# Kernel tuning notes

Measured on AMD Instinct MI355X. Metric: run time of the kernel, lower is better.

Reference implementation:

```python
import jax, jax.numpy as jnp
import numpy as np

T, N, D, E, L = 3, 50000, 64, 800000, 2


def setup_inputs() -> dict:
    key = jax.random.key(0)
    ks = jax.random.split(key, 12)
    glorot = lambda k, shape: jax.random.uniform(
        k, shape, jnp.float32, -1.0, 1.0) * np.sqrt(6.0 / (shape[-2] + shape[-1]))
    return {
        "x": jax.random.normal(ks[0], (N, D), jnp.float32),
        "edge_index": jax.random.randint(ks[1], (2, E), 0, N),
        "edge_type": jax.random.randint(ks[2], (E,), 0, T),
        "edge_feature": jax.random.normal(ks[3], (T, D), jnp.float32),
        # per-layer parameters stacked along leading L axis
        "theta_g": glorot(ks[4], (L, T, D)),
        "theta_hi": glorot(ks[5], (L, T, D)),
        "theta_hj": glorot(ks[6], (L, T, D)),
        "we": glorot(ks[7], (L, D, D)),
        "wr": glorot(ks[8], (L, D, D)),
    }


def _scatter_softmax(r, row, n):
    # r: [T,E], softmax over edges grouped by destination node `row`
    rT = r.T  # [E,T]
    m = jax.ops.segment_max(rT, row, num_segments=n)  # [N,T]
    e = jnp.exp(rT - m[row])
    s = jax.ops.segment_sum(e, row, num_segments=n)
    return (e / s[row]).T  # [T,E]


def _layer(x, ef, tg, thi, thj, we, wr, row, col, etype, n):
    # attention logits per edge, per type-slice
    r_g = jnp.einsum('ed,td->te', ef, tg)[:, etype]          # [T,E]
    r_hi = jnp.einsum('tnd,td->tn', x, thi)[:, row]          # [T,E]
    r_hj = jnp.einsum('tnd,td->tn', x, thj)[:, col]          # [T,E]
    r = _scatter_softmax(r_g + r_hi + r_hj, row, n)          # [T,E]
    ef_new = ef @ wr                                         # [et,D]
    v = jax.nn.sigmoid(ef_new)[etype][None] * (x @ we)[:, col]  # [T,E,D]
    out = r[..., None] * v                                   # [T,E,D]
    out = jax.ops.segment_sum(out.transpose(1, 0, 2), row, num_segments=n)
    return out.transpose(1, 0, 2), ef_new                    # [T,N,D]


def reference(x, edge_index, edge_type, edge_feature, theta_g, theta_hi, theta_hj, we, wr):
    row, col = edge_index[0], edge_index[1]
    h = jnp.broadcast_to(x[None], (T, N, D))
    ef = edge_feature
    for i in range(L):
        h_prev = h
        out, ef = _layer(h, ef, theta_g[i], theta_hi[i], theta_hj[i],
                         we[i], wr[i], row, col, edge_type, N)
        if i == L - 1:
            h = out
            break
        h = h_prev + jax.nn.relu(out)  # dropout p=0 -> identity
        ef = jax.nn.relu(ef)
    return h
```

## Files before the change

kernel.cpp:

```cpp
#include <hip/hip_runtime.h>
#include <math.h>

#define TT 3
#define NN 50000
#define DD 64
#define EE 800000
#define LL 2
#define NK3 (NN * TT)
#define NB3 ((NK3 + 255) / 256)
#define CH 96
#define NBC ((EE + 255) / 256)
#define NBM ((NN + 63) / 64)

typedef _Float16 h4 __attribute__((ext_vector_type(4)));
typedef float f4 __attribute__((ext_vector_type(4)));

__global__ __launch_bounds__(256) void k_fusedA(
    const int* __restrict__ row, const int* __restrict__ et,
    int* __restrict__ counts, unsigned* __restrict__ keyrank,
    const float* __restrict__ x,
    const float* __restrict__ we,
    const float* __restrict__ thj,
    _Float16* __restrict__ hw0,
    float* __restrict__ ahj0,
    const float* __restrict__ ef0,
    const float* __restrict__ tg,
    const float* __restrict__ wr,
    float* __restrict__ rg,
    float* __restrict__ sig,
    _Float16* __restrict__ bf)
{
    __shared__ _Float16 Ah[64][68];
    __shared__ _Float16 Bt[80][68];
    int b = blockIdx.x, tid = threadIdx.x;

    if (b < NBC) {
        int e = b * 256 + tid;
        if (e < EE) {
            int key = row[e] * 3 + et[e];
            int r = atomicAdd(&counts[key], 1);
            keyrank[e] = ((unsigned)key << 14) | (unsigned)r;
        }
        return;
    }
    if (b < NBC + NBM) {
        long rbase = (long)(b - NBC) * 64;
        #pragma unroll
        for (int it = 0; it < 4; ++it) {
            int flat = (tid + it * 256) * 4;
            int r = flat >> 6, k = flat & 63;
            h4 hv = {};
            if (rbase + r < NN) {
                float4 v = *(const float4*)&x[(rbase + r) * 64 + k];
                hv = h4{ (_Float16)v.x, (_Float16)v.y, (_Float16)v.z, (_Float16)v.w };
            }
            *(h4*)&Ah[r][k] = hv;
        }
        for (int idx = tid; idx < 80 * 64; idx += 256) {
            int c = idx >> 6, k = idx & 63;
            float v = 0.f;
            if (c < 64) v = we[k * 64 + c];
            else if (c < 67) v = thj[(c - 64) * 64 + k];
            Bt[c][k] = (_Float16)v;
        }
        __syncthreads();
        int wid = tid >> 6, lane = tid & 63;
        int r16 = lane & 15, kq = lane >> 4;
        f4 acc[5] = {};
        #pragma unroll
        for (int ks = 0; ks < 4; ++ks) {
            int k0 = ks * 16 + kq * 4;
            h4 a = *(h4*)&Ah[wid * 16 + r16][k0];
            #pragma unroll
            for (int ct = 0; ct < 5; ++ct) {
                h4 bb = *(h4*)&Bt[ct * 16 + r16][k0];
                acc[ct] = __builtin_amdgcn_mfma_f32_16x16x16f16(a, bb, acc[ct], 0, 0, 0);
            }
        }
        #pragma unroll
        for (int j = 0; j < 4; ++j) {
            long g = rbase + wid * 16 + kq * 4 + j;
            if (g < NN) {
                #pragma unroll
                for (int ct = 0; ct < 4; ++ct)
                    hw0[g * 64 + ct * 16 + r16] = (_Float16)acc[ct][j];
                if (r16 < 3) ahj0[g * 4 + r16] = acc[4][j];
            }
        }
        return;
    }
    float* ef_l = (float*)&Ah[0][0];
    float* efn  = ef_l + TT * DD;
    for (int l = 0; l < LL; ++l)
        for (int idx = tid; idx < 80 * 64; idx += 256) {
            int c = idx >> 6, k = idx & 63;
            float v = 0.f;
            if (c < 64) v = we[l * 4096 + k * 64 + c];
            else if (c < 67) v = thj[l * 192 + (c - 64) * 64 + k];
            bf[l * 5120 + idx] = (_Float16)v;
        }
    if (tid < TT * DD) ef_l[tid] = ef0[tid];
    __syncthreads();
    for (int layer = 0; layer < LL; ++layer) {
        if (tid < TT * TT) {
            int t = tid / TT, tau = tid % TT;
            float s = 0.f;
            #pragma unroll
            for (int k = 0; k < DD; ++k)
                s += ef_l[tau * DD + k] * tg[layer * TT * DD + t * DD + k];
            rg[layer * TT * TT + tid] = s;
        }
        if (tid < TT * DD) {
            int tau = tid / DD, d = tid % DD;
            float s = 0.f;
            #pragma unroll
            for (int k = 0; k < DD; ++k)
                s += ef_l[tau * DD + k] * wr[layer * DD * DD + k * DD + d];
            efn[tid] = s;
            sig[layer * TT * DD + tid] = 1.f / (1.f + expf(-s));
        }
        __syncthreads();
        if (tid < TT * DD) ef_l[tid] = fmaxf(efn[tid], 0.f);
        __syncthreads();
    }
}

__global__ void k_bsum(const int* __restrict__ counts, int* __restrict__ bsum)
{
    __shared__ int red[256];
    int i = blockIdx.x * 256 + threadIdx.x;
    red[threadIdx.x] = (i < NK3) ? counts[i] : 0;
    __syncthreads();
    for (int off = 128; off >= 1; off >>= 1) {
        if (threadIdx.x < off) red[threadIdx.x] += red[threadIdx.x + off];
        __syncthreads();
    }
    if (threadIdx.x == 0) bsum[blockIdx.x] = red[0];
}

__global__ void k_emit2(const int* __restrict__ counts,
                        const int* __restrict__ bsum,
                        int* __restrict__ csroff)
{
    __shared__ int s[256];
    __shared__ int bpre_s;
    int b = blockIdx.x, tid = threadIdx.x;
    int pp = 0;
    for (int i = tid; i < b; i += 256) pp += bsum[i];
    s[tid] = pp;
    __syncthreads();
    for (int off = 128; off >= 1; off >>= 1) {
        if (tid < off) s[tid] += s[tid + off];
        __syncthreads();
    }
    if (tid == 0) bpre_s = s[0];
    __syncthreads();
    int bpre = bpre_s;
    int idx = b * 256 + tid;
    int c = (idx < NK3) ? counts[idx] : 0;
    s[tid] = c;
    __syncthreads();
    for (int off = 1; off < 256; off <<= 1) {
        int u = (tid >= off) ? s[tid - off] : 0;
        __syncthreads();
        s[tid] += u;
        __syncthreads();
    }
    if (idx < NK3) csroff[idx] = bpre + s[tid] - c;
    if (b == NB3 - 1 && tid == 255) csroff[NK3] = bpre + s[255];
}

__global__ void k_scatter3r(const unsigned* __restrict__ keyrank,
                            const int* __restrict__ col,
                            const int* __restrict__ csroff,
                            unsigned short* __restrict__ pk)
{
    int e = blockIdx.x * 256 + threadIdx.x;
    if (e < EE) {
        unsigned kr = keyrank[e];
        int pos = csroff[kr >> 14] + (int)(kr & 16383u);
        pk[pos] = (unsigned short)col[e];
    }
}

__global__ __launch_bounds__(256) void k_mm1(
    const _Float16* __restrict__ h,
    const _Float16* __restrict__ Bf,
    _Float16* __restrict__ hw,
    float* __restrict__ ahj)
{
    __shared__ _Float16 Ah[64][68];
    __shared__ _Float16 Bt[80][68];
    int tid = threadIdx.x;
    long rbase = (long)blockIdx.x * 64;

    #pragma unroll
    for (int it = 0; it < 4; ++it) {
        int flat = (tid + it * 256) * 4;
        int r = flat >> 6, k = flat & 63;
        h4 hv = {};
        if (rbase + r < NK3) hv = *(const h4*)&h[(rbase + r) * 64 + k];
        *(h4*)&Ah[r][k] = hv;
    }
    for (int e4 = tid; e4 < 80 * 64 / 4; e4 += 256) {
        int idx = e4 * 4;
        *(h4*)&Bt[idx >> 6][idx & 63] = *(const h4*)&Bf[idx];
    }
    __syncthreads();

    int wid = tid >> 6, lane = tid & 63;
    int r16 = lane & 15, kq = lane >> 4;
    f4 acc[5] = {};
    #pragma unroll
    for (int ks = 0; ks < 4; ++ks) {
        int k0 = ks * 16 + kq * 4;
        h4 a = *(h4*)&Ah[wid * 16 + r16][k0];
        #pragma unroll
        for (int ct = 0; ct < 5; ++ct) {
            h4 b = *(h4*)&Bt[ct * 16 + r16][k0];
            acc[ct] = __builtin_amdgcn_mfma_f32_16x16x16f16(a, b, acc[ct], 0, 0, 0);
        }
    }
    #pragma unroll
    for (int j = 0; j < 4; ++j) {
        long g = rbase + wid * 16 + kq * 4 + j;
        if (g < NK3) {
            int t = (g >= 2L * NN) ? 2 : (g >= NN ? 1 : 0);
            long n = g - (long)t * NN;
            #pragma unroll
            for (int ct = 0; ct < 4; ++ct)
                hw[((size_t)n * 3 + t) * 64 + ct * 16 + r16] = (_Float16)acc[ct][j];
            if (r16 == t) ahj[n * 4 + t] = acc[4][j];
        }
    }
}

__global__ __launch_bounds__(256) void k_edge0(
    const int* __restrict__ off3,
    const unsigned short* __restrict__ pk,
    const float* __restrict__ rg_l,
    const float* __restrict__ sig_l,
    const float* __restrict__ ahj4,
    const _Float16* __restrict__ hw,
    const float* __restrict__ x,
    _Float16* __restrict__ outh)
{
    __shared__ uint4 ent[4][CH];
    int wid = threadIdx.x >> 6, lane = threadIdx.x & 63;
    int n = blockIdx.x * 4 + wid;
    int b3 = n * 3;
    int s0 = off3[b3], s1 = off3[b3 + 1], s2 = off3[b3 + 2], s3 = off3[b3 + 3];
    float r00 = rg_l[0], r01 = rg_l[1], r02 = rg_l[2];
    float r10 = rg_l[3], r11 = rg_l[4], r12 = rg_l[5];
    float r20 = rg_l[6], r21 = rg_l[7], r22 = rg_l[8];
    float sg0 = sig_l[lane], sg1 = sig_l[64 + lane], sg2 = sig_l[128 + lane];
    const char* hwb = (const char*)hw + (size_t)lane * 2;
    uint4* myent = ent[wid];
    float acc0 = 0.f, acc1 = 0.f, acc2 = 0.f;
    float ps0 = 0.f, ps1 = 0.f, ps2 = 0.f;

    for (int base = s0; base < s3; base += CH) {
        int cnt = s3 - base; if (cnt > CH) cnt = CH;
        for (int jj = lane; jj < cnt; jj += 64) {
            int ei = base + jj;
            int c = pk[ei];
            int tau = (ei >= s1) + (ei >= s2);
            float4 aj = *(const float4*)&ahj4[c * 4];
            float g0 = (tau == 0) ? r00 : ((tau == 1) ? r01 : r02);
            float g1 = (tau == 0) ? r10 : ((tau == 1) ? r11 : r12);
            float g2 = (tau == 0) ? r20 : ((tau == 1) ? r21 : r22);
            float p0 = __expf(g0 + aj.x);
            float p1 = __expf(g1 + aj.y);
            float p2 = __expf(g2 + aj.z);
            ps0 += p0; ps1 += p1; ps2 += p2;
            myent[jj] = make_uint4(((unsigned)c * 128u) | ((unsigned)tau << 26),
                                   __float_as_uint(p0), __float_as_uint(p1),
                                   __float_as_uint(p2));
        }
        asm volatile("s_waitcnt lgkmcnt(0)" ::: "memory");

#define AGG(J) { uint4 e = myent[J];                                           \
        unsigned ta = e.x >> 26;                                               \
        float sg = (ta == 0) ? sg0 : ((ta == 1) ? sg1 : sg2);                  \
        float sv = sg * (float)*(const _Float16*)(hwb + (e.x & 0x03FFFFFFu));  \
        acc0 = fmaf(__uint_as_float(e.y), sv, acc0);                           \
        acc1 = fmaf(__uint_as_float(e.z), sv, acc1);                           \
        acc2 = fmaf(__uint_as_float(e.w), sv, acc2); }
        int j = 0;
        for (; j + 4 <= cnt; j += 4) { AGG(j) AGG(j + 1) AGG(j + 2) AGG(j + 3) }
        for (; j < cnt; ++j) { AGG(j) }
#undef AGG
        asm volatile("s_waitcnt lgkmcnt(0)" ::: "memory");
    }
    #pragma unroll
    for (int off = 32; off >= 1; off >>= 1) {
        ps0 += __shfl_xor(ps0, off);
        ps1 += __shfl_xor(ps1, off);
        ps2 += __shfl_xor(ps2, off);
    }
    float o0 = 0.f, o1 = 0.f, o2 = 0.f;
    if (s3 > s0) { o0 = acc0 / ps0; o1 = acc1 / ps1; o2 = acc2 / ps2; }
    size_t oi = (size_t)n * 64 + lane;
    float xv = x[oi];
    outh[oi]                       = (_Float16)(xv + fmaxf(o0, 0.f));
    outh[oi + (size_t)NN * 64]     = (_Float16)(xv + fmaxf(o1, 0.f));
    outh[oi + (size_t)2 * NN * 64] = (_Float16)(xv + fmaxf(o2, 0.f));
}

__global__ __launch_bounds__(256) void k_edge1(
    const int* __restrict__ off3,
    const unsigned short* __restrict__ pk,
    const float* __restrict__ rg_l,
    const float* __restrict__ sig_l,
    const float* __restrict__ ahj4,
    const _Float16* __restrict__ hw,
    float* __restrict__ outf)
{
    __shared__ uint4 ent[4][CH];
    int wid = threadIdx.x >> 6, lane = threadIdx.x & 63;
    int n = blockIdx.x * 4 + wid;
    int b3 = n * 3;
    int s0 = off3[b3], s1 = off3[b3 + 1], s2 = off3[b3 + 2], s3 = off3[b3 + 3];
    float r00 = rg_l[0], r01 = rg_l[1], r02 = rg_l[2];
    float r10 = rg_l[3], r11 = rg_l[4], r12 = rg_l[5];
    float r20 = rg_l[6], r21 = rg_l[7], r22 = rg_l[8];
    float sg0 = sig_l[lane], sg1 = sig_l[64 + lane], sg2 = sig_l[128 + lane];
    const char* hwb = (const char*)hw + (size_t)lane * 2;
    uint4* myent = ent[wid];
    float acc0 = 0.f, acc1 = 0.f, acc2 = 0.f;
    float ps0 = 0.f, ps1 = 0.f, ps2 = 0.f;

    for (int base = s0; base < s3; base += CH) {
        int cnt = s3 - base; if (cnt > CH) cnt = CH;
        for (int jj = lane; jj < cnt; jj += 64) {
            int ei = base + jj;
            int c = pk[ei];
            int tau = (ei >= s1) + (ei >= s2);
            float4 aj = *(const float4*)&ahj4[c * 4];
            float g0 = (tau == 0) ? r00 : ((tau == 1) ? r01 : r02);
            float g1 = (tau == 0) ? r10 : ((tau == 1) ? r11 : r12);
            float g2 = (tau == 0) ? r20 : ((tau == 1) ? r21 : r22);
            float p0 = __expf(g0 + aj.x);
            float p1 = __expf(g1 + aj.y);
            float p2 = __expf(g2 + aj.z);
            ps0 += p0; ps1 += p1; ps2 += p2;
            myent[jj] = make_uint4(((unsigned)c * 384u) | ((unsigned)tau << 26),
                                   __float_as_uint(p0), __float_as_uint(p1),
                                   __float_as_uint(p2));
        }
        asm volatile("s_waitcnt lgkmcnt(0)" ::: "memory");

#define AGG(J) { uint4 e = myent[J];                                           \
        unsigned ta = e.x >> 26;                                               \
        float sg = (ta == 0) ? sg0 : ((ta == 1) ? sg1 : sg2);                  \
        const char* ptr = hwb + (e.x & 0x03FFFFFFu);                           \
        float v0 = (float)*(const _Float16*)(ptr);                             \
        float v1 = (float)*(const _Float16*)(ptr + 128);                       \
        float v2 = (float)*(const _Float16*)(ptr + 256);                       \
        acc0 = fmaf(__uint_as_float(e.y), sg * v0, acc0);                      \
        acc1 = fmaf(__uint_as_float(e.z), sg * v1, acc1);                      \
        acc2 = fmaf(__uint_as_float(e.w), sg * v2, acc2); }
        int j = 0;
        for (; j + 4 <= cnt; j += 4) { AGG(j) AGG(j + 1) AGG(j + 2) AGG(j + 3) }
        for (; j < cnt; ++j) { AGG(j) }
#undef AGG
        asm volatile("s_waitcnt lgkmcnt(0)" ::: "memory");
    }
    #pragma unroll
    for (int off = 32; off >= 1; off >>= 1) {
        ps0 += __shfl_xor(ps0, off);
        ps1 += __shfl_xor(ps1, off);
        ps2 += __shfl_xor(ps2, off);
    }
    float o0 = 0.f, o1 = 0.f, o2 = 0.f;
    if (s3 > s0) { o0 = acc0 / ps0; o1 = acc1 / ps1; o2 = acc2 / ps2; }
    size_t oi = (size_t)n * 64 + lane;
    outf[oi]                       = o0;
    outf[oi + (size_t)NN * 64]     = o1;
    outf[oi + (size_t)2 * NN * 64] = o2;
}

extern "C" void kernel_launch(void* const* d_in, const int* in_sizes, int n_in,
                              void* d_out, int out_size, void* d_ws, size_t ws_size,
                              hipStream_t stream)
{
    const float* x   = (const float*)d_in[0];
    const int*   ei  = (const int*)d_in[1];
    const int*   row = ei;
    const int*   col = ei + EE;
    const int*   et  = (const int*)d_in[2];
    const float* ef  = (const float*)d_in[3];
    const float* tg  = (const float*)d_in[4];
    const float* thj = (const float*)d_in[6];
    const float* we  = (const float*)d_in[7];
    const float* wr  = (const float*)d_in[8];
    float* out = (float*)d_out;
    _Float16* h1h = (_Float16*)d_out;

    _Float16* hw1 = (_Float16*)d_ws;
    _Float16* hw0 = hw1 + (size_t)NN * 3 * 64;
    float* ahj0 = (float*)(hw0 + (size_t)NN * 64);
    float* ahj1 = ahj0 + (size_t)NN * 4;
    float* rg   = ahj1 + (size_t)NN * 4;
    float* sig  = rg + LL * 9;
    _Float16* bfB = (_Float16*)(sig + LL * 192);
    int* counts3 = (int*)(bfB + LL * 5120);
    int* csroff3 = counts3 + NK3;
    int* bsum    = csroff3 + NK3 + 1;
    unsigned* keyrank = (unsigned*)(bsum + NB3);
    unsigned short* csrpk = (unsigned short*)(keyrank + EE);

    hipMemsetAsync(counts3, 0, NK3 * sizeof(int), stream);
    k_fusedA<<<NBC + NBM + 1, 256, 0, stream>>>(row, et, counts3, keyrank,
                                                x, we, thj, hw0, ahj0,
                                                ef, tg, wr, rg, sig, bfB);
    k_bsum<<<NB3, 256, 0, stream>>>(counts3, bsum);
    k_emit2<<<NB3, 256, 0, stream>>>(counts3, bsum, csroff3);
    k_scatter3r<<<(EE + 255) / 256, 256, 0, stream>>>(keyrank, col, csroff3, csrpk);
    k_edge0<<<NN / 4, 256, 0, stream>>>(csroff3, csrpk, rg, sig, ahj0, hw0,
                                        x, h1h);
    k_mm1<<<(NK3 + 63) / 64, 256, 0, stream>>>(h1h, bfB + 5120, hw1, ahj1);
    k_edge1<<<NN / 4, 256, 0, stream>>>(csroff3, csrpk, rg + 9, sig + 192,
                                        ahj1, hw1, out);
}
```

Before: 173.5 us.

## Replace global-atomic CSR build with two-level bucketed counting sort

Replaces the per-key global atomic counting, the block-sum scan and the rank-based scatter with a two-level radix-style sort. Edges are first bucketed by row/128 using shared-memory histograms and a transposed per-block offset table, then each bucket is locally sorted by (row,type) key in shared memory to emit CSR offsets and column indices. The intent is to avoid heavily contended global atomics and scattered writes. The cost is extra passes, serial in-block scans over 3125 blocks per bucket column, and the removal of the memset.

After: 170.3 us. About the same (-1.9%).

```diff
diff --git a/kernel.cpp b/kernel.cpp
--- a/kernel.cpp
+++ b/kernel.cpp
@@ -7,17 +7,19 @@
 #define EE 800000
 #define LL 2
 #define NK3 (NN * TT)
-#define NB3 ((NK3 + 255) / 256)
 #define CH 96
 #define NBC ((EE + 255) / 256)
 #define NBM ((NN + 63) / 64)
+#define NBKT ((NN + 127) / 128)
+#define KPB 384
+#define HP 3136
 
 typedef _Float16 h4 __attribute__((ext_vector_type(4)));
 typedef float f4 __attribute__((ext_vector_type(4)));
 
 __global__ __launch_bounds__(256) void k_fusedA(
     const int* __restrict__ row, const int* __restrict__ et,
-    int* __restrict__ counts, unsigned* __restrict__ keyrank,
+    int* __restrict__ blockHistT,
     const float* __restrict__ x,
     const float* __restrict__ we,
     const float* __restrict__ thj,
@@ -32,15 +34,18 @@
 {
     __shared__ _Float16 Ah[64][68];
     __shared__ _Float16 Bt[80][68];
+    __shared__ int lhist[NBKT];
     int b = blockIdx.x, tid = threadIdx.x;
 
     if (b < NBC) {
+        for (int i = tid; i < NBKT; i += 256) lhist[i] = 0;
+        __syncthreads();
         int e = b * 256 + tid;
-        if (e < EE) {
-            int key = row[e] * 3 + et[e];
-            int r = atomicAdd(&counts[key], 1);
-            keyrank[e] = ((unsigned)key << 14) | (unsigned)r;
-        }
+        int bkt = row[e] >> 7;
+        atomicAdd(&lhist[bkt], 1);
+        __syncthreads();
+        for (int i = tid; i < NBKT; i += 256)
+            blockHistT[(size_t)i * HP + b] = lhist[i];
         return;
     }
     if (b < NBC + NBM) {
@@ -125,61 +130,134 @@
     }
 }
 
-__global__ void k_bsum(const int* __restrict__ counts, int* __restrict__ bsum)
-{
-    __shared__ int red[256];
-    int i = blockIdx.x * 256 + threadIdx.x;
-    red[threadIdx.x] = (i < NK3) ? counts[i] : 0;
+__global__ __launch_bounds__(256) void k_colscan(
+    int* __restrict__ blockHistT, int* __restrict__ bucketTotal)
+{
+    __shared__ int sc[256];
+    __shared__ int carryB;
+    int j = blockIdx.x, tid = threadIdx.x;
+    int* colp = blockHistT + (size_t)j * HP;
+    if (tid == 0) carryB = 0;
+    __syncthreads();
+    for (int c0 = 0; c0 < NBC; c0 += 256) {
+        int b = c0 + tid;
+        int v = (b < NBC) ? colp[b] : 0;
+        sc[tid] = v;
+        __syncthreads();
+        for (int off = 1; off < 256; off <<= 1) {
+            int u = (tid >= off) ? sc[tid - off] : 0;
+            __syncthreads();
+            sc[tid] += u;
+            __syncthreads();
+        }
+        int cb = carryB;
+        if (b < NBC) colp[b] = cb + sc[tid] - v;
+        __syncthreads();
+        if (tid == 0) carryB = cb + sc[255];
+        __syncthreads();
+    }
+    if (tid == 0) bucketTotal[j] = carryB;
+}
+
+__global__ __launch_bounds__(256) void k_bucket(
+    const int* __restrict__ row, const int* __restrict__ et,
+    const int* __restrict__ col,
+    const int* __restrict__ bucketTotal,
+    const int* __restrict__ blockOffT,
+    unsigned* __restrict__ bucketed)
+{
+    __shared__ int lrank[NBKT];
+    __shared__ int lbase[NBKT];
+    __shared__ int sc[256];
+    __shared__ int carryC;
+    int b = blockIdx.x, tid = threadIdx.x;
+    for (int i = tid; i < NBKT; i += 256) lrank[i] = 0;
+    if (tid == 0) carryC = 0;
+    __syncthreads();
+    for (int c0 = 0; c0 < NBKT; c0 += 256) {
+        int i = c0 + tid;
+        int v = (i < NBKT) ? bucketTotal[i] : 0;
+        sc[tid] = v;
+        __syncthreads();
+        for (int off = 1; off < 256; off <<= 1) {
+            int u = (tid >= off) ? sc[tid - off] : 0;
+            __syncthreads();
+            sc[tid] += u;
+            __syncthreads();
+        }
+        int cb = carryC;
+        if (i < NBKT) lbase[i] = cb + sc[tid] - v;
+        __syncthreads();
+        if (tid == 0) carryC = cb + sc[255];
+        __syncthreads();
+    }
+    int e = b * 256 + tid;
+    int r = row[e], tt = et[e], c = col[e];
+    int bkt = r >> 7;
+    int kl = (r - (bkt << 7)) * 3 + tt;
+    int rk = atomicAdd(&lrank[bkt], 1);
+    int pos = lbase[bkt] + blockOffT[(size_t)bkt * HP + b] + rk;
+    bucketed[pos] = ((unsigned)kl << 16) | (unsigned)c;
+}
+
+__global__ __launch_bounds__(256) void k_emit3(
+    const unsigned* __restrict__ bucketed,
+    const int* __restrict__ bucketTotal,
+    int* __restrict__ csroff,
+    unsigned short* __restrict__ pk)
+{
+    __shared__ int counts[KPB];
+    __shared__ int csr[KPB];
+    __shared__ int sc[256];
+    __shared__ int carryS;
+    int j = blockIdx.x, tid = threadIdx.x;
+    int pp = 0;
+    for (int i = tid; i < j; i += 256) pp += bucketTotal[i];
+    sc[tid] = pp;
     __syncthreads();
     for (int off = 128; off >= 1; off >>= 1) {
-        if (threadIdx.x < off) red[threadIdx.x] += red[threadIdx.x + off];
-        __syncthreads();
-    }
-    if (threadIdx.x == 0) bsum[blockIdx.x] = red[0];
-}
-
-__global__ void k_emit2(const int* __restrict__ counts,
-                        const int* __restrict__ bsum,
-                        int* __restrict__ csroff)
-{
-    __shared__ int s[256];
-    __shared__ int bpre_s;
-    int b = blockIdx.x, tid = threadIdx.x;
-    int pp = 0;
-    for (int i = tid; i < b; i += 256) pp += bsum[i];
-    s[tid] = pp;
-    __syncthreads();
-    for (int off = 128; off >= 1; off >>= 1) {
-        if (tid < off) s[tid] += s[tid + off];
-        __syncthreads();
-    }
-    if (tid == 0) bpre_s = s[0];
-    __syncthreads();
-    int bpre = bpre_s;
-    int idx = b * 256 + tid;
-    int c = (idx < NK3) ? counts[idx] : 0;
-    s[tid] = c;
-    __syncthreads();
-    for (int off = 1; off < 256; off <<= 1) {
-        int u = (tid >= off) ? s[tid - off] : 0;
-        __syncthreads();
-        s[tid] += u;
-        __syncthreads();
-    }
-    if (idx < NK3) csroff[idx] = bpre + s[tid] - c;
-    if (b == NB3 - 1 && tid == 255) csroff[NK3] = bpre + s[255];
-}
-
-__global__ void k_scatter3r(const unsigned* __restrict__ keyrank,
-                            const int* __restrict__ col,
-                            const int* __restrict__ csroff,
-                            unsigned short* __restrict__ pk)
-{
-    int e = blockIdx.x * 256 + threadIdx.x;
-    if (e < EE) {
-        unsigned kr = keyrank[e];
-        int pos = csroff[kr >> 14] + (int)(kr & 16383u);
-        pk[pos] = (unsigned short)col[e];
+        if (tid < off) sc[tid] += sc[tid + off];
+        __syncthreads();
+    }
+    int base = sc[0];
+    int tot = bucketTotal[j];
+    __syncthreads();
+    for (int k = tid; k < KPB; k += 256) counts[k] = 0;
+    if (tid == 0) carryS = 0;
+    __syncthreads();
+    for (int i = tid; i < tot; i += 256) {
+        int kl = (int)(bucketed[base + i] >> 16);
+        atomicAdd(&counts[kl], 1);
+    }
+    __syncthreads();
+    for (int c0 = 0; c0 < KPB; c0 += 256) {
+        int k = c0 + tid;
+        int v = (k < KPB) ? counts[k] : 0;
+        sc[tid] = v;
+        __syncthreads();
+        for (int off = 1; off < 256; off <<= 1) {
+            int u = (tid >= off) ? sc[tid - off] : 0;
+            __syncthreads();
+            sc[tid] += u;
+            __syncthreads();
+        }
+        int cb = carryS;
+        if (k < KPB) csr[k] = cb + sc[tid] - v;
+        __syncthreads();
+        if (tid == 0) carryS = cb + sc[255];
+        __syncthreads();
+    }
+    for (int k = tid; k < KPB; k += 256) {
+        int gk = j * KPB + k;
+        if (gk <= NK3) csroff[gk] = base + csr[k];
+    }
+    for (int k = tid; k < KPB; k += 256) counts[k] = 0;
+    __syncthreads();
+    for (int i = tid; i < tot; i += 256) {
+        unsigned rec = bucketed[base + i];
+        int kl = (int)(rec >> 16);
+        int rk = atomicAdd(&counts[kl], 1);
+        pk[base + csr[kl] + rk] = (unsigned short)(rec & 0xFFFFu);
     }
 }
 
@@ -404,19 +482,20 @@
     float* rg   = ahj1 + (size_t)NN * 4;
     float* sig  = rg + LL * 9;
     _Float16* bfB = (_Float16*)(sig + LL * 192);
-    int* counts3 = (int*)(bfB + LL * 5120);
-    int* csroff3 = counts3 + NK3;
-    int* bsum    = csroff3 + NK3 + 1;
-    unsigned* keyrank = (unsigned*)(bsum + NB3);
-    unsigned short* csrpk = (unsigned short*)(keyrank + EE);
-
-    hipMemsetAsync(counts3, 0, NK3 * sizeof(int), stream);
-    k_fusedA<<<NBC + NBM + 1, 256, 0, stream>>>(row, et, counts3, keyrank,
+    int* csroff3 = (int*)(bfB + LL * 5120);
+    int* bucketTotal = csroff3 + NK3 + 1;
+    int* blockHistT  = bucketTotal + NBKT;
+    unsigned* bucketed = (unsigned*)(blockHistT + (size_t)NBKT * HP);
+    unsigned short* csrpk = (unsigned short*)(bucketed + EE);
+
+    k_fusedA<<<NBC + NBM + 1, 256, 0, stream>>>(row, et, blockHistT,
                                                 x, we, thj, hw0, ahj0,
                                                 ef, tg, wr, rg, sig, bfB);
-    k_bsum<<<NB3, 256, 0, stream>>>(counts3, bsum);
-    k_emit2<<<NB3, 256, 0, stream>>>(counts3, bsum, csroff3);
-    k_scatter3r<<<(EE + 255) / 256, 256, 0, stream>>>(keyrank, col, csroff3, csrpk);
+    k_colscan<<<NBKT, 256, 0, stream>>>(blockHistT, bucketTotal);
+    k_bucket<<<NBC, 256, 0, stream>>>(row, et, col, bucketTotal, blockHistT,
+                                      bucketed);
+    k_emit3<<<NBKT, 256, 0, stream>>>(bucketed, bucketTotal, csroff3, csrpk);
+
     k_edge0<<<NN / 4, 256, 0, stream>>>(csroff3, csrpk, rg, sig, ahj0, hw0,
                                         x, h1h);
     k_mm1<<<(NK3 + 63) / 64, 256, 0, stream>>>(h1h, bfB + 5120, hw1, ahj1);
```
